# Optimization experiments

Measured on AMD Instinct MI355X. Metric: run time of the kernel, lower is better.

Reference implementation:

```python
import jax, jax.numpy as jnp
import numpy as np

# ---- constants mirroring the torch module ----
LOSS_ALPHA = 1.0      # args.loss_weight_alpha (intra-class weight)
LOSS_BETA = 1.0       # args.loss_weight_beta (focal weight)
FOCAL_GAMMA = 2.0
FOCAL_ALPHA = 0.85
EPS = 1e-09
LDAM_S = 30.0
CLS_NUM = np.array([85.0, 900.0])
LDAM_MAX_M = 0.5
LDAM_W = np.array([0.15, 0.85], dtype=np.float32)
B = 16777216


def setup_inputs() -> dict:
    key = jax.random.key(0)
    k1, k2 = jax.random.split(key)
    x = jax.random.uniform(k1, (B, 2), dtype=jnp.float32)  # [B, 2] probabilities-like logits
    target = jax.random.randint(k2, (B,), 0, 2)            # binary labels
    return {"x": x, "target": target}


def _intraclass_p(centered, std, target, cls):
    # correlation between consecutive same-class rows (sorted-index order),
    # vectorized: class-c indices first via stable argsort, mask invalid pairs.
    n_rows = centered.shape[0]
    mask = target == cls
    n = jnp.sum(mask)
    order = jnp.argsort(jnp.where(mask, jnp.arange(n_rows), n_rows))
    a, b = order[:-1], order[1:]
    corr = jnp.sum(centered[a] * centered[b], axis=1) / (std[a] * std[b])
    valid = jnp.arange(n_rows - 1) < (n - 1)
    s = jnp.sum(jnp.where(valid, corr, 0.0))
    return jnp.where(n > 0, s / jnp.maximum(n, 1).astype(s.dtype), 0.0)


def reference(x, target):
    num_cls = x.shape[1]
    # ---- LDAM loss ----
    m = 1.0 / np.sqrt(np.sqrt(CLS_NUM))
    m = m * (LDAM_MAX_M / np.max(m))
    m_list = jnp.asarray(m, jnp.float32)
    w = jnp.asarray(LDAM_W)
    batch_m = m_list[target]                                      # [B]
    onehot = jax.nn.one_hot(target, num_cls, dtype=bool)          # [B, C]
    out = jnp.where(onehot, x - batch_m[:, None], x)              # margin on target logit only
    logsm = jax.nn.log_softmax(LDAM_S * out, axis=-1)
    nll = -jnp.take_along_axis(logsm, target[:, None], axis=1)[:, 0]
    wi = w[target]
    ldam = jnp.sum(wi * nll) / jnp.sum(wi)                        # weighted-mean cross entropy
    # ---- binary focal loss (treats x[:,1] as probability) ----
    p = x[:, 1]
    t = target.astype(x.dtype)
    fl = (-FOCAL_ALPHA * t * (1.0 - p) ** FOCAL_GAMMA * jnp.log(p + EPS)
          - (1.0 - FOCAL_ALPHA) * (1.0 - t) * p ** FOCAL_GAMMA * jnp.log(1.0 - p + EPS))
    focal = jnp.mean(fl)
    # ---- intra-class correlation loss ----
    centered = x - jnp.mean(x, axis=1, keepdims=True)
    std = jnp.std(x, axis=1, ddof=1)                               # torch.std default: unbiased
    p0 = _intraclass_p(centered, std, target, 0)
    p1 = _intraclass_p(centered, std, target, 1)
    intra = (p0 - p1) ** 2
    return ldam + LOSS_BETA * focal + LOSS_ALPHA * intra
```

## Files before the change

### kernel.cpp

```cpp
#include <hip/hip_runtime.h>

#define E_BLOCK 8192
#define E_WAVE  2048
#define QITERS  8

#define M1f     0.2771814156f
#define C_A1    60.0f
#define C_C1    (30.0f*M1f - 15.0f)

#define EXP2F(v) __builtin_amdgcn_exp2f(v)
#define LOG2F(v) __builtin_amdgcn_logf(v)

struct BlockRec {
  int s0, p0, s1, p1;
  float wnll, fl;
  int cnt1, pad;
};

__device__ __forceinline__ void comb0(int &s, int &f, int &l, int sb, int fb, int lb) {
  s += sb + l * fb;
  f = f ? f : fb;
  l = fb ? lb : l;
}

__device__ __forceinline__ void bfly_step(int m, int lane, int &s, int &f, int &l) {
  const int os = __shfl_xor(s, m), of = __shfl_xor(f, m), ol = __shfl_xor(l, m);
  const bool up = (lane & m) != 0;
  int as = up ? os : s, af = up ? of : f, al = up ? ol : l;
  const int bs = up ? s : os, bf = up ? f : of, bl = up ? l : ol;
  comb0(as, af, al, bs, bf, bl);
  s = as; f = af; l = al;
}

__device__ __forceinline__ void elem_math(float x0, float x1, int t, int k,
                                          float &wnll, float &flraw, int &cnt1,
                                          unsigned int &word) {
  const float tf  = (float)t;
  const float wgt = fmaf(tf, 0.7f, 0.15f);
  const float d   = x0 - x1;
  const float za  = fmaf(tf, C_A1, -30.0f);
  const float zc  = fmaf(tf, C_C1, 15.0f);
  const float z   = fmaf(za, d, zc);
  const float ex  = EXP2F(fabsf(z) * -1.44269504f);
  const float lp  = LOG2F(1.0f + ex);
  const float sp  = fmaf(0.69314718f, lp, fmaxf(z, 0.0f));
  wnll = fmaf(wgt, sp, wnll);
  const float om  = 1.0f - x1;
  const float q   = t ? x1 : om;
  const float r   = t ? om : x1;
  const float lg2 = LOG2F(q + 1e-9f);
  const float wr2 = (wgt * r) * r;
  flraw = fmaf(wr2, lg2, flraw);
  cnt1 += t;
  const unsigned int code = 4u | (unsigned int)(d > 0.0f) | ((unsigned int)t << 1);
  word |= code << (8 * k);
}

__global__ __launch_bounds__(256, 2) void loss_pass1(
    const float* __restrict__ x, const int* __restrict__ tgt,
    BlockRec* __restrict__ recs, int B) {
  __shared__ unsigned int lds[3328];
  unsigned int* chunkw = lds;
  unsigned int* stw = lds + 2304;
  float* wnw = (float*)(lds + 2560);
  float* flw = (float*)(lds + 2816);
  int*   cnw = (int*)(lds + 3072);

  const int tid = threadIdx.x;
  const int w = tid >> 6, lane = tid & 63;
  const int waveBase = blockIdx.x * E_BLOCK + w * E_WAVE;

  float wnll = 0.f, flraw = 0.f; int cnt1 = 0;

  if (waveBase + E_WAVE <= B) {
    const int e0 = waveBase + lane * 4;
    const float4* __restrict__ px = (const float4*)(x + 2 * (size_t)e0);
    const int4*   __restrict__ pt = (const int4*)(tgt + e0);

    float4 xa[QITERS], xb[QITERS]; int4 t4[QITERS];
    #pragma unroll
    for (int j = 0; j < QITERS; ++j) {
      xa[j] = px[j * 128];
      xb[j] = px[j * 128 + 1];
      t4[j] = pt[j * 64];
    }
    #pragma unroll
    for (int j = 0; j < QITERS; ++j) {
      unsigned int word = 0;
      elem_math(xa[j].x, xa[j].y, t4[j].x, 0, wnll, flraw, cnt1, word);
      elem_math(xa[j].z, xa[j].w, t4[j].y, 1, wnll, flraw, cnt1, word);
      elem_math(xb[j].x, xb[j].y, t4[j].z, 2, wnll, flraw, cnt1, word);
      elem_math(xb[j].z, xb[j].w, t4[j].w, 3, wnll, flraw, cnt1, word);
      const int qi = w * 512 + (j << 6) + lane;
      chunkw[(qi >> 3) * 9 + (qi & 7)] = word;
    }
  } else {
    for (int j = 0; j < QITERS; ++j) {
      unsigned int word = 0;
      for (int k = 0; k < 4; ++k) {
        const int e = waveBase + ((j << 6) + lane) * 4 + k;
        if (e < B) {
          elem_math(x[2 * (size_t)e], x[2 * (size_t)e + 1], tgt[e], k,
                    wnll, flraw, cnt1, word);
        }
      }
      const int qi = w * 512 + (j << 6) + lane;
      chunkw[(qi >> 3) * 9 + (qi & 7)] = word;
    }
  }
  __syncthreads();

  int s0 = 0, f0 = 0, l0 = 0, s1 = 0, f1 = 0, l1 = 0;
  #pragma unroll
  for (int r = 0; r < 8; ++r) {
    const unsigned int wv = chunkw[tid * 9 + r];
    #pragma unroll
    for (int k = 0; k < 4; ++k) {
      const unsigned int b = (wv >> (8 * k)) & 7u;
      if (b & 4u) {
        const int sv = (int)((b & 1u) << 1) - 1;
        const int t  = (int)((b >> 1) & 1u);
        const int lv = t ? l1 : l0;
        const int add = lv * sv;
        if (t) { s1 += add; l1 = sv; f1 = f1 ? f1 : sv; }
        else   { s0 += add; l0 = sv; f0 = f0 ? f0 : sv; }
      }
    }
  }
  stw[tid] = (unsigned)(s0 + 128) | ((unsigned)(f0 + 1) << 8) | ((unsigned)(l0 + 1) << 10)
           | ((unsigned)(s1 + 128) << 16) | ((unsigned)(f1 + 1) << 24) | ((unsigned)(l1 + 1) << 26);
  wnw[tid] = wnll; flw[tid] = flraw * -0.69314718f; cnw[tid] = cnt1;
  __syncthreads();

  if (w == 0) {
    int S0 = 0, F0 = 0, L0 = 0, S1 = 0, F1 = 0, L1 = 0;
    float W = 0.f, F = 0.f; int C = 0;
    #pragma unroll
    for (int q = 0; q < 4; ++q) {
      const int i = lane * 4 + q;
      const unsigned int pk = stw[i];
      comb0(S0, F0, L0, (int)(pk & 255u) - 128, (int)((pk >> 8) & 3u) - 1, (int)((pk >> 10) & 3u) - 1);
      comb0(S1, F1, L1, (int)((pk >> 16) & 255u) - 128, (int)((pk >> 24) & 3u) - 1, (int)((pk >> 26) & 3u) - 1);
      W += wnw[i]; F += flw[i]; C += cnw[i];
    }
    #pragma unroll
    for (int k = 0; k < 6; ++k) {
      const int m = 1 << k;
      bfly_step(m, lane, S0, F0, L0);
      bfly_step(m, lane, S1, F1, L1);
      W += __shfl_xor(W, m); F += __shfl_xor(F, m); C += __shfl_xor(C, m);
    }
    if (lane == 0) {
      BlockRec r;
      r.s0 = S0; r.p0 = (F0 + 1) | ((L0 + 1) << 4);
      r.s1 = S1; r.p1 = (F1 + 1) | ((L1 + 1) << 4);
      r.wnll = W; r.fl = F; r.cnt1 = C; r.pad = 0;
      recs[blockIdx.x] = r;
    }
  }
}

__global__ __launch_bounds__(256) void loss_pass2(
    const BlockRec* __restrict__ recs, int NB, int B, float* __restrict__ out) {
  __shared__ int sS0[256], sF0[256], sL0[256], sS1[256], sF1[256], sL1[256], sC[256];
  __shared__ double sW[256], sFl[256];
  const int tid = threadIdx.x, w = tid >> 6, lane = tid & 63;
  const int R = (NB + 255) >> 8;

  int s0 = 0, f0 = 0, l0 = 0, s1 = 0, f1 = 0, l1 = 0;
  double W = 0.0, Fd = 0.0; int C = 0;
  for (int r = 0; r < R; ++r) {
    const int b = tid * R + r;
    if (b < NB) {
      const BlockRec rec = recs[b];
      comb0(s0, f0, l0, rec.s0, (rec.p0 & 3) - 1, ((rec.p0 >> 4) & 3) - 1);
      comb0(s1, f1, l1, rec.s1, (rec.p1 & 3) - 1, ((rec.p1 >> 4) & 3) - 1);
      W += (double)rec.wnll; Fd += (double)rec.fl; C += rec.cnt1;
    }
  }
  sS0[tid] = s0; sF0[tid] = f0; sL0[tid] = l0;
  sS1[tid] = s1; sF1[tid] = f1; sL1[tid] = l1;
  sC[tid] = C; sW[tid] = W; sFl[tid] = Fd;
  __syncthreads();

  if (w == 0) {
    int S0 = 0, F0 = 0, L0 = 0, S1 = 0, F1 = 0, L1 = 0; int Ct = 0;
    double Wt = 0.0, Ft = 0.0;
    #pragma unroll
    for (int q = 0; q < 4; ++q) {
      const int i = lane * 4 + q;
      comb0(S0, F0, L0, sS0[i], sF0[i], sL0[i]);
      comb0(S1, F1, L1, sS1[i], sF1[i], sL1[i]);
      Wt += sW[i]; Ft += sFl[i]; Ct += sC[i];
    }
    #pragma unroll
    for (int k = 0; k < 6; ++k) {
      const int m = 1 << k;
      bfly_step(m, lane, S0, F0, L0);
      bfly_step(m, lane, S1, F1, L1);
      Wt += __shfl_xor(Wt, m); Ft += __shfl_xor(Ft, m); Ct += __shfl_xor(Ct, m);
    }
    if (lane == 0) {
      const double n1 = (double)Ct, n0 = (double)B - n1;
      const double sw = 0.15 * n0 + 0.85 * n1;
      const double ldam  = Wt / sw;
      const double focal = Ft / (double)B;
      const double q0 = (n0 > 0.0) ? (double)S0 / n0 : 0.0;
      const double q1 = (n1 > 0.0) ? (double)S1 / n1 : 0.0;
      const double dq = q0 - q1;
      out[0] = (float)(ldam + focal + dq * dq);
    }
  }
}

extern "C" void kernel_launch(void* const* d_in, const int* in_sizes, int n_in,
                              void* d_out, int out_size, void* d_ws, size_t ws_size,
                              hipStream_t stream) {
  const float* x  = (const float*)d_in[0];
  const int* tgt  = (const int*)d_in[1];
  float* out      = (float*)d_out;
  const int B  = in_sizes[1];
  const int NB = (B + E_BLOCK - 1) / E_BLOCK;
  BlockRec* recs = (BlockRec*)d_ws;
  loss_pass1<<<NB, 256, 0, stream>>>(x, tgt, recs, B);
  loss_pass2<<<1, 256, 0, stream>>>(recs, NB, B, out);
}
```

Baseline: 241.3 us.

## Halve per-block work and software-pipeline loads with double-buffered registers

```diff
diff --git a/kernel.cpp b/kernel.cpp
--- a/kernel.cpp
+++ b/kernel.cpp
@@ -1,8 +1,8 @@
 #include <hip/hip_runtime.h>
 
-#define E_BLOCK 8192
-#define E_WAVE  2048
-#define QITERS  8
+#define E_BLOCK 4096
+#define E_WAVE  1024
+#define QITERS  4
 
 #define M1f     0.2771814156f
 #define C_A1    60.0f
@@ -56,15 +56,15 @@
   word |= code << (8 * k);
 }
 
-__global__ __launch_bounds__(256, 2) void loss_pass1(
+__global__ __launch_bounds__(256, 8) void loss_pass1(
     const float* __restrict__ x, const int* __restrict__ tgt,
     BlockRec* __restrict__ recs, int B) {
-  __shared__ unsigned int lds[3328];
+  __shared__ unsigned int lds[2304];
   unsigned int* chunkw = lds;
-  unsigned int* stw = lds + 2304;
-  float* wnw = (float*)(lds + 2560);
-  float* flw = (float*)(lds + 2816);
-  int*   cnw = (int*)(lds + 3072);
+  unsigned int* stw = lds + 1280;
+  float* wnw = (float*)(lds + 1536);
+  float* flw = (float*)(lds + 1792);
+  int*   cnw = (int*)(lds + 2048);
 
   const int tid = threadIdx.x;
   const int w = tid >> 6, lane = tid & 63;
@@ -77,22 +77,46 @@
     const float4* __restrict__ px = (const float4*)(x + 2 * (size_t)e0);
     const int4*   __restrict__ pt = (const int4*)(tgt + e0);
 
-    float4 xa[QITERS], xb[QITERS]; int4 t4[QITERS];
-    #pragma unroll
-    for (int j = 0; j < QITERS; ++j) {
-      xa[j] = px[j * 128];
-      xb[j] = px[j * 128 + 1];
-      t4[j] = pt[j * 64];
-    }
-    #pragma unroll
-    for (int j = 0; j < QITERS; ++j) {
-      unsigned int word = 0;
-      elem_math(xa[j].x, xa[j].y, t4[j].x, 0, wnll, flraw, cnt1, word);
-      elem_math(xa[j].z, xa[j].w, t4[j].y, 1, wnll, flraw, cnt1, word);
-      elem_math(xb[j].x, xb[j].y, t4[j].z, 2, wnll, flraw, cnt1, word);
-      elem_math(xb[j].z, xb[j].w, t4[j].w, 3, wnll, flraw, cnt1, word);
-      const int qi = w * 512 + (j << 6) + lane;
-      chunkw[(qi >> 3) * 9 + (qi & 7)] = word;
+    float4 aA = px[0];   float4 bA = px[1];   int4 tA = pt[0];
+    float4 aB = px[128]; float4 bB = px[129]; int4 tB = pt[64];
+
+    {
+      unsigned int word = 0;
+      elem_math(aA.x, aA.y, tA.x, 0, wnll, flraw, cnt1, word);
+      elem_math(aA.z, aA.w, tA.y, 1, wnll, flraw, cnt1, word);
+      elem_math(bA.x, bA.y, tA.z, 2, wnll, flraw, cnt1, word);
+      elem_math(bA.z, bA.w, tA.w, 3, wnll, flraw, cnt1, word);
+      const int qi = w * 256 + lane;
+      chunkw[(qi >> 2) * 5 + (qi & 3)] = word;
+    }
+    aA = px[256]; bA = px[257]; tA = pt[128];
+    {
+      unsigned int word = 0;
+      elem_math(aB.x, aB.y, tB.x, 0, wnll, flraw, cnt1, word);
+      elem_math(aB.z, aB.w, tB.y, 1, wnll, flraw, cnt1, word);
+      elem_math(bB.x, bB.y, tB.z, 2, wnll, flraw, cnt1, word);
+      elem_math(bB.z, bB.w, tB.w, 3, wnll, flraw, cnt1, word);
+      const int qi = w * 256 + 64 + lane;
+      chunkw[(qi >> 2) * 5 + (qi & 3)] = word;
+    }
+    aB = px[384]; bB = px[385]; tB = pt[192];
+    {
+      unsigned int word = 0;
+      elem_math(aA.x, aA.y, tA.x, 0, wnll, flraw, cnt1, word);
+      elem_math(aA.z, aA.w, tA.y, 1, wnll, flraw, cnt1, word);
+      elem_math(bA.x, bA.y, tA.z, 2, wnll, flraw, cnt1, word);
+      elem_math(bA.z, bA.w, tA.w, 3, wnll, flraw, cnt1, word);
+      const int qi = w * 256 + 128 + lane;
+      chunkw[(qi >> 2) * 5 + (qi & 3)] = word;
+    }
+    {
+      unsigned int word = 0;
+      elem_math(aB.x, aB.y, tB.x, 0, wnll, flraw, cnt1, word);
+      elem_math(aB.z, aB.w, tB.y, 1, wnll, flraw, cnt1, word);
+      elem_math(bB.x, bB.y, tB.z, 2, wnll, flraw, cnt1, word);
+      elem_math(bB.z, bB.w, tB.w, 3, wnll, flraw, cnt1, word);
+      const int qi = w * 256 + 192 + lane;
+      chunkw[(qi >> 2) * 5 + (qi & 3)] = word;
     }
   } else {
     for (int j = 0; j < QITERS; ++j) {
@@ -104,16 +128,16 @@
                     wnll, flraw, cnt1, word);
         }
       }
-      const int qi = w * 512 + (j << 6) + lane;
-      chunkw[(qi >> 3) * 9 + (qi & 7)] = word;
+      const int qi = w * 256 + (j << 6) + lane;
+      chunkw[(qi >> 2) * 5 + (qi & 3)] = word;
     }
   }
   __syncthreads();
 
   int s0 = 0, f0 = 0, l0 = 0, s1 = 0, f1 = 0, l1 = 0;
   #pragma unroll
-  for (int r = 0; r < 8; ++r) {
-    const unsigned int wv = chunkw[tid * 9 + r];
+  for (int r = 0; r < 4; ++r) {
+    const unsigned int wv = chunkw[tid * 5 + r];
     #pragma unroll
     for (int k = 0; k < 4; ++k) {
       const unsigned int b = (wv >> (8 * k)) & 7u;
```

New measurement: 243.2 us. Within noise of the previous version (+0.8%).

## Shrink blocks to four elements per thread and fold sign scan inline

Applied to the files above, without the earlier changes.

```diff
diff --git a/kernel.cpp b/kernel.cpp
--- a/kernel.cpp
+++ b/kernel.cpp
@@ -1,8 +1,6 @@
 #include <hip/hip_runtime.h>
 
-#define E_BLOCK 8192
-#define E_WAVE  2048
-#define QITERS  8
+#define E_BLOCK 1024
 
 #define M1f     0.2771814156f
 #define C_A1    60.0f
@@ -10,12 +8,6 @@
 
 #define EXP2F(v) __builtin_amdgcn_exp2f(v)
 #define LOG2F(v) __builtin_amdgcn_logf(v)
-
-struct BlockRec {
-  int s0, p0, s1, p1;
-  float wnll, fl;
-  int cnt1, pad;
-};
 
 __device__ __forceinline__ void comb0(int &s, int &f, int &l, int sb, int fb, int lb) {
   s += sb + l * fb;
@@ -32,9 +24,9 @@
   s = as; f = af; l = al;
 }
 
-__device__ __forceinline__ void elem_math(float x0, float x1, int t, int k,
-                                          float &wnll, float &flraw, int &cnt1,
-                                          unsigned int &word) {
+__device__ __forceinline__ void elem_all(float x0, float x1, int t,
+    float &wnll, float &flraw, int &cnt1,
+    int &s0, int &f0, int &l0, int &s1, int &f1, int &l1) {
   const float tf  = (float)t;
   const float wgt = fmaf(tf, 0.7f, 0.15f);
   const float d   = x0 - x1;
@@ -52,81 +44,47 @@
   const float wr2 = (wgt * r) * r;
   flraw = fmaf(wr2, lg2, flraw);
   cnt1 += t;
-  const unsigned int code = 4u | (unsigned int)(d > 0.0f) | ((unsigned int)t << 1);
-  word |= code << (8 * k);
+  const int sv = (d > 0.0f) ? 1 : -1;
+  const int lv = t ? l1 : l0;
+  const int add = lv * sv;
+  if (t) { s1 += add; l1 = sv; f1 = f1 ? f1 : sv; }
+  else   { s0 += add; l0 = sv; f0 = f0 ? f0 : sv; }
 }
 
-__global__ __launch_bounds__(256, 2) void loss_pass1(
+__global__ __launch_bounds__(256) void loss_pass1(
     const float* __restrict__ x, const int* __restrict__ tgt,
-    BlockRec* __restrict__ recs, int B) {
-  __shared__ unsigned int lds[3328];
-  unsigned int* chunkw = lds;
-  unsigned int* stw = lds + 2304;
-  float* wnw = (float*)(lds + 2560);
-  float* flw = (float*)(lds + 2816);
-  int*   cnw = (int*)(lds + 3072);
+    int4* __restrict__ recs, int B) {
+  __shared__ unsigned int stw[256];
+  __shared__ float wnw[256];
+  __shared__ float flw[256];
+  __shared__ int   cnw[256];
 
   const int tid = threadIdx.x;
   const int w = tid >> 6, lane = tid & 63;
-  const int waveBase = blockIdx.x * E_BLOCK + w * E_WAVE;
+  const int base = blockIdx.x * E_BLOCK + tid * 4;
 
   float wnll = 0.f, flraw = 0.f; int cnt1 = 0;
+  int s0 = 0, f0 = 0, l0 = 0, s1 = 0, f1 = 0, l1 = 0;
 
-  if (waveBase + E_WAVE <= B) {
-    const int e0 = waveBase + lane * 4;
-    const float4* __restrict__ px = (const float4*)(x + 2 * (size_t)e0);
-    const int4*   __restrict__ pt = (const int4*)(tgt + e0);
-
-    float4 xa[QITERS], xb[QITERS]; int4 t4[QITERS];
-    #pragma unroll
-    for (int j = 0; j < QITERS; ++j) {
-      xa[j] = px[j * 128];
-      xb[j] = px[j * 128 + 1];
-      t4[j] = pt[j * 64];
-    }
-    #pragma unroll
-    for (int j = 0; j < QITERS; ++j) {
-      unsigned int word = 0;
-      elem_math(xa[j].x, xa[j].y, t4[j].x, 0, wnll, flraw, cnt1, word);
-      elem_math(xa[j].z, xa[j].w, t4[j].y, 1, wnll, flraw, cnt1, word);
-      elem_math(xb[j].x, xb[j].y, t4[j].z, 2, wnll, flraw, cnt1, word);
-      elem_math(xb[j].z, xb[j].w, t4[j].w, 3, wnll, flraw, cnt1, word);
-      const int qi = w * 512 + (j << 6) + lane;
-      chunkw[(qi >> 3) * 9 + (qi & 7)] = word;
-    }
+  if (base + 4 <= B) {
+    const float4* __restrict__ px = (const float4*)(x + 2 * (size_t)base);
+    const float4 a = px[0];
+    const float4 b = px[1];
+    const int4  t4 = *(const int4*)(tgt + base);
+    elem_all(a.x, a.y, t4.x, wnll, flraw, cnt1, s0, f0, l0, s1, f1, l1);
+    elem_all(a.z, a.w, t4.y, wnll, flraw, cnt1, s0, f0, l0, s1, f1, l1);
+    elem_all(b.x, b.y, t4.z, wnll, flraw, cnt1, s0, f0, l0, s1, f1, l1);
+    elem_all(b.z, b.w, t4.w, wnll, flraw, cnt1, s0, f0, l0, s1, f1, l1);
   } else {
-    for (int j = 0; j < QITERS; ++j) {
-      unsigned int word = 0;
-      for (int k = 0; k < 4; ++k) {
-        const int e = waveBase + ((j << 6) + lane) * 4 + k;
-        if (e < B) {
-          elem_math(x[2 * (size_t)e], x[2 * (size_t)e + 1], tgt[e], k,
-                    wnll, flraw, cnt1, word);
-        }
-      }
-      const int qi = w * 512 + (j << 6) + lane;
-      chunkw[(qi >> 3) * 9 + (qi & 7)] = word;
-    }
-  }
-  __syncthreads();
-
-  int s0 = 0, f0 = 0, l0 = 0, s1 = 0, f1 = 0, l1 = 0;
-  #pragma unroll
-  for (int r = 0; r < 8; ++r) {
-    const unsigned int wv = chunkw[tid * 9 + r];
-    #pragma unroll
     for (int k = 0; k < 4; ++k) {
-      const unsigned int b = (wv >> (8 * k)) & 7u;
-      if (b & 4u) {
-        const int sv = (int)((b & 1u) << 1) - 1;
-        const int t  = (int)((b >> 1) & 1u);
-        const int lv = t ? l1 : l0;
-        const int add = lv * sv;
-        if (t) { s1 += add; l1 = sv; f1 = f1 ? f1 : sv; }
-        else   { s0 += add; l0 = sv; f0 = f0 ? f0 : sv; }
+      const int e = base + k;
+      if (e < B) {
+        elem_all(x[2 * (size_t)e], x[2 * (size_t)e + 1], tgt[e],
+                 wnll, flraw, cnt1, s0, f0, l0, s1, f1, l1);
       }
     }
   }
+
   stw[tid] = (unsigned)(s0 + 128) | ((unsigned)(f0 + 1) << 8) | ((unsigned)(l0 + 1) << 10)
            | ((unsigned)(s1 + 128) << 16) | ((unsigned)(f1 + 1) << 24) | ((unsigned)(l1 + 1) << 26);
   wnw[tid] = wnll; flw[tid] = flraw * -0.69314718f; cnw[tid] = cnt1;
@@ -151,17 +109,20 @@
       W += __shfl_xor(W, m); F += __shfl_xor(F, m); C += __shfl_xor(C, m);
     }
     if (lane == 0) {
-      BlockRec r;
-      r.s0 = S0; r.p0 = (F0 + 1) | ((L0 + 1) << 4);
-      r.s1 = S1; r.p1 = (F1 + 1) | ((L1 + 1) << 4);
-      r.wnll = W; r.fl = F; r.cnt1 = C; r.pad = 0;
-      recs[blockIdx.x] = r;
+      int4 rv;
+      rv.x = (int)(((unsigned)(S0 + 1024) & 0xFFFFu) | ((unsigned)(S1 + 1024) << 16));
+      rv.y = (int)((unsigned)(F0 + 1) | ((unsigned)(L0 + 1) << 2)
+                 | ((unsigned)(F1 + 1) << 4) | ((unsigned)(L1 + 1) << 6)
+                 | ((unsigned)C << 8));
+      rv.z = __float_as_int(W);
+      rv.w = __float_as_int(F);
+      recs[blockIdx.x] = rv;
     }
   }
 }
 
 __global__ __launch_bounds__(256) void loss_pass2(
-    const BlockRec* __restrict__ recs, int NB, int B, float* __restrict__ out) {
+    const int4* __restrict__ recs, int NB, int B, float* __restrict__ out) {
   __shared__ int sS0[256], sF0[256], sL0[256], sS1[256], sF1[256], sL1[256], sC[256];
   __shared__ double sW[256], sFl[256];
   const int tid = threadIdx.x, w = tid >> 6, lane = tid & 63;
@@ -169,13 +130,17 @@
 
   int s0 = 0, f0 = 0, l0 = 0, s1 = 0, f1 = 0, l1 = 0;
   double W = 0.0, Fd = 0.0; int C = 0;
+  #pragma unroll 4
   for (int r = 0; r < R; ++r) {
     const int b = tid * R + r;
     if (b < NB) {
-      const BlockRec rec = recs[b];
-      comb0(s0, f0, l0, rec.s0, (rec.p0 & 3) - 1, ((rec.p0 >> 4) & 3) - 1);
-      comb0(s1, f1, l1, rec.s1, (rec.p1 & 3) - 1, ((rec.p1 >> 4) & 3) - 1);
-      W += (double)rec.wnll; Fd += (double)rec.fl; C += rec.cnt1;
+      const int4 rv = recs[b];
+      const unsigned u0 = (unsigned)rv.x, u1 = (unsigned)rv.y;
+      comb0(s0, f0, l0, (int)(u0 & 0xFFFFu) - 1024, (int)(u1 & 3u) - 1, (int)((u1 >> 2) & 3u) - 1);
+      comb0(s1, f1, l1, (int)(u0 >> 16) - 1024, (int)((u1 >> 4) & 3u) - 1, (int)((u1 >> 6) & 3u) - 1);
+      W  += (double)__int_as_float(rv.z);
+      Fd += (double)__int_as_float(rv.w);
+      C  += (int)(u1 >> 8);
     }
   }
   sS0[tid] = s0; sF0[tid] = f0; sL0[tid] = l0;
@@ -221,7 +186,7 @@
   float* out      = (float*)d_out;
   const int B  = in_sizes[1];
   const int NB = (B + E_BLOCK - 1) / E_BLOCK;
-  BlockRec* recs = (BlockRec*)d_ws;
+  int4* recs = (int4*)d_ws;
   loss_pass1<<<NB, 256, 0, stream>>>(x, tgt, recs, B);
   loss_pass2<<<1, 256, 0, stream>>>(recs, NB, B, out);
 }
```

Result: no change. 244.2 us (+1.2%).
